# Kernel optimization log

Hardware: AMD Instinct MI355X
Metric: run time of the kernel (lower is better)

The kernel has to match this reference:

```python
import jax, jax.numpy as jnp
import numpy as np

D_IN = 1024
D_OUT = 1024


def setup_inputs() -> dict:
    key = jax.random.key(0)
    kx, kq, kk, kv = jax.random.split(key, 4)
    s = 1.0 / np.sqrt(D_IN)
    x = jax.random.normal(kx, (2, 4096, D_IN), dtype=jnp.float32)
    # nn.Linear weights: shape [d_out, d_in], y = x @ W.T (no bias)
    W_query = jax.random.normal(kq, (D_OUT, D_IN), dtype=jnp.float32) * s
    W_key = jax.random.normal(kk, (D_OUT, D_IN), dtype=jnp.float32) * s
    W_value = jax.random.normal(kv, (D_OUT, D_IN), dtype=jnp.float32) * s
    return {"x": x, "W_query": W_query, "W_key": W_key, "W_value": W_value}


def reference(x, W_query, W_key, W_value):
    # QKV projections: [b, n, d_in] @ [d_in, d_out]
    q = jnp.einsum('bnd,od->bno', x, W_query)
    k = jnp.einsum('bnd,od->bno', x, W_key)
    v = jnp.einsum('bnd,od->bno', x, W_value)
    d_k = k.shape[-1]
    scores = jnp.einsum('bqo,bko->bqk', q, k) / jnp.sqrt(jnp.asarray(d_k, x.dtype))
    # NOTE: source applies no causal mask despite the class name
    attn = jax.nn.softmax(scores, axis=-1)
    return jnp.einsum('bqk,bko->bqo', attn, v)
```

## Files before the change

kernel.cpp:

```cpp
#include <hip/hip_runtime.h>
#include <hip/hip_bf16.h>
#include <hip/hip_fp16.h>
#include <stdint.h>

typedef __bf16 bf16_t;
typedef __bf16 bf16x8 __attribute__((ext_vector_type(8)));
typedef float f32x4 __attribute__((ext_vector_type(4)));

typedef __attribute__((address_space(1))) void gv_t;
typedef __attribute__((address_space(3))) void lv_t;

__device__ inline unsigned short f2bf_bits(float f) {
  uint32_t u = __float_as_uint(f);
  u += 0x7FFFu + ((u >> 16) & 1u);
  return (unsigned short)(u >> 16);
}
__device__ inline bf16_t f2bf(float f) {
  unsigned short h = f2bf_bits(f);
  return __builtin_bit_cast(bf16_t, h);
}

__device__ inline void storeC(float* p, float v) { *p = v; }
__device__ inline void storeC(bf16_t* p, float v) { *p = f2bf(v); }
__device__ inline void storeC(__half* p, float v) { *p = __float2half(v); }

__global__ __launch_bounds__(256)
void convert_all(const float* __restrict__ x, const float* __restrict__ wq,
                 const float* __restrict__ wk, const float* __restrict__ wv,
                 bf16_t* __restrict__ xb, bf16_t* __restrict__ wqkb,
                 bf16_t* __restrict__ wvb)
{
  const int64_t NX = 8192LL * 1024, NW = 1024LL * 1024;
  const int64_t total4 = (NX + 3 * NW) >> 2;
  for (int64_t i = (int64_t)blockIdx.x * blockDim.x + threadIdx.x; i < total4;
       i += (int64_t)gridDim.x * blockDim.x) {
    int64_t e = i << 2;
    const float* src; bf16_t* dst; int64_t off;
    if (e < NX)               { src = x;  dst = xb;         off = e; }
    else if (e < NX + NW)     { src = wq; dst = wqkb;       off = e - NX; }
    else if (e < NX + 2 * NW) { src = wk; dst = wqkb + NW;  off = e - NX - NW; }
    else                      { src = wv; dst = wvb;        off = e - NX - 2 * NW; }
    float4 f = *(const float4*)(src + off);
    uint32_t lo = ((uint32_t)f2bf_bits(f.y) << 16) | f2bf_bits(f.x);
    uint32_t hi = ((uint32_t)f2bf_bits(f.w) << 16) | f2bf_bits(f.z);
    *(uint2*)(dst + off) = make_uint2(lo, hi);
  }
}

template <typename OUT_T>
__global__ __launch_bounds__(256)
void gemm_bt(const bf16_t* __restrict__ A, const bf16_t* __restrict__ B,
             OUT_T* __restrict__ C, int K, int lda, int ldb, int ldc,
             int64_t b_batch_stride, int bm_per_batch)
{
  __shared__ bf16_t As[2][128 * 32];
  __shared__ bf16_t Bs[2][128 * 32];
  const int tid  = threadIdx.x;
  const int wid  = tid >> 6;
  const int lane = tid & 63;
  const int wm = wid >> 1, wn = wid & 1;
  const int64_t bm = blockIdx.x;
  const int64_t bn = blockIdx.y;

  const bf16_t* Bb = B + (bm / bm_per_batch) * b_batch_stride;

  const int c0row = (wid * 2 + 0) * 16 + (lane >> 2);
  const int c1row = (wid * 2 + 1) * 16 + (lane >> 2);
  const int scol  = (lane & 3) * 8;

  const bf16_t* Ar0 = A  + (bm * 128 + c0row) * lda + scol;
  const bf16_t* Ar1 = A  + (bm * 128 + c1row) * lda + scol;
  const bf16_t* Br0 = Bb + (bn * 128 + c0row) * ldb + scol;
  const bf16_t* Br1 = Bb + (bn * 128 + c1row) * ldb + scol;

  const int ad0 = (wid * 2 + 0) * 512;
  const int ad1 = (wid * 2 + 1) * 512;

  const int frow = lane & 15;
  const int fk   = (lane >> 4) * 8;
  const int aoff = (wm * 64 + frow) * 32 + fk;
  const int boff = (wn * 64 + frow) * 32 + fk;

  f32x4 acc[4][4];
  #pragma unroll
  for (int m = 0; m < 4; m++)
    #pragma unroll
    for (int n = 0; n < 4; n++) acc[m][n] = f32x4{0.f, 0.f, 0.f, 0.f};

  auto stage = [&](int buf, int k0) {
    __builtin_amdgcn_global_load_lds((const gv_t*)(Ar0 + k0),
                                     (lv_t*)(&As[buf][ad0]), 16, 0, 0);
    __builtin_amdgcn_global_load_lds((const gv_t*)(Ar1 + k0),
                                     (lv_t*)(&As[buf][ad1]), 16, 0, 0);
    __builtin_amdgcn_global_load_lds((const gv_t*)(Br0 + k0),
                                     (lv_t*)(&Bs[buf][ad0]), 16, 0, 0);
    __builtin_amdgcn_global_load_lds((const gv_t*)(Br1 + k0),
                                     (lv_t*)(&Bs[buf][ad1]), 16, 0, 0);
  };

  stage(0, 0);
  __syncthreads();
  int cur = 0;
  for (int k0 = 0; k0 < K; k0 += 32) {
    if (k0 + 32 < K) stage(cur ^ 1, k0 + 32);

    bf16x8 af[4], bfr[4];
    #pragma unroll
    for (int m = 0; m < 4; m++)
      af[m] = *(const bf16x8*)(&As[cur][aoff + m * 16 * 32]);
    #pragma unroll
    for (int n = 0; n < 4; n++)
      bfr[n] = *(const bf16x8*)(&Bs[cur][boff + n * 16 * 32]);
    #pragma unroll
    for (int m = 0; m < 4; m++)
      #pragma unroll
      for (int n = 0; n < 4; n++)
        acc[m][n] = __builtin_amdgcn_mfma_f32_16x16x32_bf16(af[m], bfr[n],
                                                            acc[m][n], 0, 0, 0);
    __syncthreads();
    cur ^= 1;
  }

  const int crow = (lane >> 4) * 4;
  const int ccol = lane & 15;
  #pragma unroll
  for (int m = 0; m < 4; m++)
    #pragma unroll
    for (int n = 0; n < 4; n++)
      #pragma unroll
      for (int j = 0; j < 4; j++) {
        int64_t row = bm * 128 + wm * 64 + m * 16 + crow + j;
        int64_t col = bn * 128 + wn * 64 + n * 16 + ccol;
        storeC(&C[row * ldc + col], acc[m][n][j]);
      }
}

template <typename OUT_T>
__global__ __launch_bounds__(512, 2)
void gemm256(const bf16_t* __restrict__ A, const bf16_t* __restrict__ B,
             OUT_T* __restrict__ C0, OUT_T* __restrict__ C1,
             int K, int lda, int ldb, int ldc,
             int64_t b_batch_stride, int bm_per_batch,
             int64_t za_off, int64_t zb_off)
{
  __shared__ bf16_t As[2][256][64];
  __shared__ bf16_t Bs[2][256][64];

  const int tid  = threadIdx.x;
  const int wid  = tid >> 6;
  const int lane = tid & 63;
  const int wm = wid >> 2;
  const int wn = wid & 3;
  const int64_t bm = blockIdx.x;
  const int64_t bn = blockIdx.y;
  const int z = blockIdx.z;

  OUT_T* __restrict__ C = (z == 0) ? C0 : C1;
  const bf16_t* Ap = A + (int64_t)z * za_off;
  const bf16_t* Bp = B + (bm / bm_per_batch) * b_batch_stride
                       + (int64_t)z * zb_off;

  const int srow  = wid * 16 + (lane >> 3);
  const int sslot = (lane & 7) ^ (lane >> 3);
  const int64_t lda64 = lda, ldb64 = ldb;
  const bf16_t* Ag = Ap + (bm * 256 + srow) * lda64 + sslot * 8;
  const bf16_t* Bg = Bp + (bn * 256 + srow) * ldb64 + sslot * 8;

  auto stageA = [&](int buf, int t, int h) {
    const bf16_t* src = Ag + (int64_t)(h * 128) * lda64 + t * 64;
    char* dst = (char*)&As[buf][h * 128 + wid * 16][0];
    __builtin_amdgcn_global_load_lds((const gv_t*)src, (lv_t*)dst, 16, 0, 0);
    __builtin_amdgcn_global_load_lds((const gv_t*)(src + 8 * lda64),
                                     (lv_t*)(dst + 1024), 16, 0, 0);
  };
  auto stageB = [&](int buf, int t, int h) {
    const bf16_t* src = Bg + (int64_t)(h * 128) * ldb64 + t * 64;
    char* dst = (char*)&Bs[buf][h * 128 + wid * 16][0];
    __builtin_amdgcn_global_load_lds((const gv_t*)src, (lv_t*)dst, 16, 0, 0);
    __builtin_amdgcn_global_load_lds((const gv_t*)(src + 8 * ldb64),
                                     (lv_t*)(dst + 1024), 16, 0, 0);
  };

  const int frow   = lane & 15;
  const int fcol16 = lane >> 4;
  const int xorv   = (lane & 7) << 4;
  const int ck0 = (fcol16 * 16) ^ xorv;
  const int ck1 = (64 + fcol16 * 16) ^ xorv;
  const int arowb = (wm * 128 + frow) * 128;
  const int browb = (wn * 64  + frow) * 128;

  f32x4 acc[8][4];
  #pragma unroll
  for (int m = 0; m < 8; m++)
    #pragma unroll
    for (int n = 0; n < 4; n++) acc[m][n] = f32x4{0.f, 0.f, 0.f, 0.f};

  const int NT = K >> 6;

  stageA(0, 0, 0); stageA(0, 0, 1);
  stageB(0, 0, 0); stageB(0, 0, 1);
  stageB(1, 1, 0); stageB(1, 1, 1);
  asm volatile("s_waitcnt vmcnt(4)" ::: "memory");
  __builtin_amdgcn_s_barrier();
  __builtin_amdgcn_sched_barrier(0);

  bf16x8 a[4][2], bb[4][2];

  for (int g = 0; g < NT; ++g) {
    const int buf = g & 1;
    const char* lA = (const char*)&As[buf][0][0];
    const char* lB = (const char*)&Bs[buf][0][0];

    #pragma unroll
    for (int m = 0; m < 4; m++) {
      a[m][0] = *(const bf16x8*)(lA + arowb + m * 2048 + ck0);
      a[m][1] = *(const bf16x8*)(lA + arowb + m * 2048 + ck1);
    }
    #pragma unroll
    for (int n = 0; n < 2; n++) {
      bb[n][0] = *(const bf16x8*)(lB + browb + n * 2048 + ck0);
      bb[n][1] = *(const bf16x8*)(lB + browb + n * 2048 + ck1);
    }
    if (g + 1 < NT) stageA(buf ^ 1, g + 1, 0);
    __builtin_amdgcn_s_barrier();
    __builtin_amdgcn_s_setprio(1);
    #pragma unroll
    for (int m = 0; m < 4; m++)
      #pragma unroll
      for (int n = 0; n < 2; n++)
        #pragma unroll
        for (int k = 0; k < 2; k++)
          acc[m][n] = __builtin_amdgcn_mfma_f32_16x16x32_bf16(a[m][k], bb[n][k],
                                                              acc[m][n], 0, 0, 0);
    __builtin_amdgcn_s_setprio(0);
    __builtin_amdgcn_s_barrier();

    #pragma unroll
    for (int n = 2; n < 4; n++) {
      bb[n][0] = *(const bf16x8*)(lB + browb + n * 2048 + ck0);
      bb[n][1] = *(const bf16x8*)(lB + browb + n * 2048 + ck1);
    }
    if (g + 1 < NT) stageA(buf ^ 1, g + 1, 1);
    __builtin_amdgcn_s_barrier();
    __builtin_amdgcn_s_setprio(1);
    #pragma unroll
    for (int m = 0; m < 4; m++)
      #pragma unroll
      for (int n = 2; n < 4; n++)
        #pragma unroll
        for (int k = 0; k < 2; k++)
          acc[m][n] = __builtin_amdgcn_mfma_f32_16x16x32_bf16(a[m][k], bb[n][k],
                                                              acc[m][n], 0, 0, 0);
    __builtin_amdgcn_s_setprio(0);
    __builtin_amdgcn_s_barrier();

    #pragma unroll
    for (int m = 0; m < 4; m++) {
      a[m][0] = *(const bf16x8*)(lA + arowb + (m + 4) * 2048 + ck0);
      a[m][1] = *(const bf16x8*)(lA + arowb + (m + 4) * 2048 + ck1);
    }
    if (g + 2 < NT) stageB(buf, g + 2, 0);
    __builtin_amdgcn_s_barrier();
    __builtin_amdgcn_s_setprio(1);
    #pragma unroll
    for (int m = 0; m < 4; m++)
      #pragma unroll
      for (int n = 0; n < 2; n++)
        #pragma unroll
        for (int k = 0; k < 2; k++)
          acc[m + 4][n] = __builtin_amdgcn_mfma_f32_16x16x32_bf16(
              a[m][k], bb[n][k], acc[m + 4][n], 0, 0, 0);
    __builtin_amdgcn_s_setprio(0);
    __builtin_amdgcn_s_barrier();

    if (g + 2 < NT) stageB(buf, g + 2, 1);
    __builtin_amdgcn_s_barrier();
    __builtin_amdgcn_s_setprio(1);
    #pragma unroll
    for (int m = 0; m < 4; m++)
      #pragma unroll
      for (int n = 2; n < 4; n++)
        #pragma unroll
        for (int k = 0; k < 2; k++)
          acc[m + 4][n] = __builtin_amdgcn_mfma_f32_16x16x32_bf16(
              a[m][k], bb[n][k], acc[m + 4][n], 0, 0, 0);
    __builtin_amdgcn_s_setprio(0);
    if (g + 2 < NT) {
      asm volatile("s_waitcnt vmcnt(4)" ::: "memory");
    } else {
      asm volatile("s_waitcnt vmcnt(0)" ::: "memory");
    }
    __builtin_amdgcn_s_barrier();
    __builtin_amdgcn_sched_barrier(0);
  }

  const int crow = (lane >> 4) * 4;
  const int ccol = lane & 15;
  #pragma unroll
  for (int m = 0; m < 8; m++)
    #pragma unroll
    for (int n = 0; n < 4; n++)
      #pragma unroll
      for (int j = 0; j < 4; j++) {
        int64_t row = bm * 256 + wm * 128 + m * 16 + crow + j;
        int64_t col = bn * 256 + wn * 64 + n * 16 + ccol;
        storeC(&C[row * (int64_t)ldc + col], acc[m][n][j]);
      }
}

__global__ __launch_bounds__(256)
void softmax_rows(__half* __restrict__ SP)
{
  const int64_t row = blockIdx.x;
  __half* s = SP + row * 4096;
  bf16_t* p = (bf16_t*)s;
  const int tid = threadIdx.x;
  const float scale = 0.03125f;

  float v[16];
  float vmax = -3.4e38f;
  #pragma unroll
  for (int i = 0; i < 4; i++) {
    uint2 raw = *(const uint2*)(s + i * 1024 + tid * 4);
    __half2 h01 = __builtin_bit_cast(__half2, raw.x);
    __half2 h23 = __builtin_bit_cast(__half2, raw.y);
    float2 f01 = __half22float2(h01);
    float2 f23 = __half22float2(h23);
    v[i * 4 + 0] = f01.x * scale;
    v[i * 4 + 1] = f01.y * scale;
    v[i * 4 + 2] = f23.x * scale;
    v[i * 4 + 3] = f23.y * scale;
    vmax = fmaxf(vmax, fmaxf(fmaxf(v[i*4+0], v[i*4+1]),
                             fmaxf(v[i*4+2], v[i*4+3])));
  }
  #pragma unroll
  for (int o = 32; o > 0; o >>= 1) vmax = fmaxf(vmax, __shfl_xor(vmax, o));
  __shared__ float redm[4];
  __shared__ float reds[4];
  if ((tid & 63) == 0) redm[tid >> 6] = vmax;
  __syncthreads();
  vmax = fmaxf(fmaxf(redm[0], redm[1]), fmaxf(redm[2], redm[3]));

  float lsum = 0.f;
  #pragma unroll
  for (int i = 0; i < 16; i++) {
    v[i] = __expf(v[i] - vmax);
    lsum += v[i];
  }
  #pragma unroll
  for (int o = 32; o > 0; o >>= 1) lsum += __shfl_xor(lsum, o);
  if ((tid & 63) == 0) reds[tid >> 6] = lsum;
  __syncthreads();
  lsum = (reds[0] + reds[1]) + (reds[2] + reds[3]);
  const float inv = 1.0f / lsum;

  #pragma unroll
  for (int i = 0; i < 4; i++) {
    uint32_t lo = ((uint32_t)f2bf_bits(v[i*4+1] * inv) << 16) | f2bf_bits(v[i*4+0] * inv);
    uint32_t hi = ((uint32_t)f2bf_bits(v[i*4+3] * inv) << 16) | f2bf_bits(v[i*4+2] * inv);
    *(uint2*)(p + i * 1024 + tid * 4) = make_uint2(lo, hi);
  }
}

__global__ __launch_bounds__(256)
void addk_f4(float4* __restrict__ o, const float4* __restrict__ a, int64_t n4)
{
  for (int64_t i = (int64_t)blockIdx.x * blockDim.x + threadIdx.x; i < n4;
       i += (int64_t)gridDim.x * blockDim.x) {
    float4 x = o[i];
    float4 y = a[i];
    x.x += y.x; x.y += y.y; x.z += y.z; x.w += y.w;
    o[i] = x;
  }
}

extern "C" void kernel_launch(void* const* d_in, const int* in_sizes, int n_in,
                              void* d_out, int out_size, void* d_ws, size_t ws_size,
                              hipStream_t stream) {
  const float* x  = (const float*)d_in[0];
  const float* wq = (const float*)d_in[1];
  const float* wk = (const float*)d_in[2];
  const float* wv = (const float*)d_in[3];
  float* out = (float*)d_out;

  char* ws = (char*)d_ws;
  bf16_t* xb   = (bf16_t*)ws;
  bf16_t* wqkb = (bf16_t*)(ws + (16LL << 20));
  bf16_t* wvb  = (bf16_t*)(ws + (20LL << 20));
  __half* S    = (__half*)ws;
  bf16_t* qk   = (bf16_t*)(ws + (64LL << 20));
  float*  pk   = (float*)(ws + (64LL << 20));
  bf16_t* vt   = (bf16_t*)(ws + (96LL << 20));

  const int NO_BATCH = 1 << 30;

  convert_all<<<2048, 256, 0, stream>>>(x, wq, wk, wv, xb, wqkb, wvb);

  gemm256<bf16_t><<<dim3(32, 8, 1), 512, 0, stream>>>(
      xb, wqkb, qk, qk, 1024, 1024, 1024, 2048, 0, NO_BATCH, 0, 0);

  gemm_bt<bf16_t><<<dim3(8, 64), 256, 0, stream>>>(
      wvb, xb, vt, 1024, 1024, 1024, 8192, 0, NO_BATCH);

  gemm256<__half><<<dim3(32, 16, 1), 512, 0, stream>>>(
      qk, qk + 1024, S, S, 1024, 2048, 2048, 4096, 4096LL * 2048, 16, 0, 0);

  softmax_rows<<<8192, 256, 0, stream>>>(S);

  gemm256<float><<<dim3(32, 4, 2), 512, 0, stream>>>(
      (const bf16_t*)S, vt, out, pk, 2048, 4096, 8192, 1024,
      4096, 16, 2048, 2048);

  addk_f4<<<2048, 256, 0, stream>>>((float4*)out, (const float4*)pk,
                                    8192LL * 1024 / 4);
}
```

Baseline: 249.0 us.

## Hoist all LDS fragment loads per k-step and store split-K partial as fp16

Each gemm256 k-iteration now loads all eight A fragments and all four B fragments from LDS at the start, instead of interleaving smaller loads between MFMA phases. This doubles the fragment registers held per thread but removes mid-iteration LDS waits. Separately, the second split-K partial of the PV GEMM is written as fp16 rather than fp32, and the reduction kernel converts it back. That halves that buffer's write and read traffic at the cost of some precision in the partial sum.

```diff
diff --git a/kernel.cpp b/kernel.cpp
--- a/kernel.cpp
+++ b/kernel.cpp
@@ -135,10 +135,10 @@
       }
 }
 
-template <typename OUT_T>
+template <typename OUT_T, typename OUT2_T>
 __global__ __launch_bounds__(512, 2)
 void gemm256(const bf16_t* __restrict__ A, const bf16_t* __restrict__ B,
-             OUT_T* __restrict__ C0, OUT_T* __restrict__ C1,
+             OUT_T* __restrict__ C0, OUT2_T* __restrict__ C1,
              int K, int lda, int ldb, int ldc,
              int64_t b_batch_stride, int bm_per_batch,
              int64_t za_off, int64_t zb_off)
@@ -155,7 +155,6 @@
   const int64_t bn = blockIdx.y;
   const int z = blockIdx.z;
 
-  OUT_T* __restrict__ C = (z == 0) ? C0 : C1;
   const bf16_t* Ap = A + (int64_t)z * za_off;
   const bf16_t* Bp = B + (bm / bm_per_batch) * b_batch_stride
                        + (int64_t)z * zb_off;
@@ -204,7 +203,7 @@
   __builtin_amdgcn_s_barrier();
   __builtin_amdgcn_sched_barrier(0);
 
-  bf16x8 a[4][2], bb[4][2];
+  bf16x8 a[8][2], bb[4][2];
 
   for (int g = 0; g < NT; ++g) {
     const int buf = g & 1;
@@ -212,12 +211,12 @@
     const char* lB = (const char*)&Bs[buf][0][0];
 
     #pragma unroll
-    for (int m = 0; m < 4; m++) {
+    for (int m = 0; m < 8; m++) {
       a[m][0] = *(const bf16x8*)(lA + arowb + m * 2048 + ck0);
       a[m][1] = *(const bf16x8*)(lA + arowb + m * 2048 + ck1);
     }
     #pragma unroll
-    for (int n = 0; n < 2; n++) {
+    for (int n = 0; n < 4; n++) {
       bb[n][0] = *(const bf16x8*)(lB + browb + n * 2048 + ck0);
       bb[n][1] = *(const bf16x8*)(lB + browb + n * 2048 + ck1);
     }
@@ -235,11 +234,6 @@
     __builtin_amdgcn_s_setprio(0);
     __builtin_amdgcn_s_barrier();
 
-    #pragma unroll
-    for (int n = 2; n < 4; n++) {
-      bb[n][0] = *(const bf16x8*)(lB + browb + n * 2048 + ck0);
-      bb[n][1] = *(const bf16x8*)(lB + browb + n * 2048 + ck1);
-    }
     if (g + 1 < NT) stageA(buf ^ 1, g + 1, 1);
     __builtin_amdgcn_s_barrier();
     __builtin_amdgcn_s_setprio(1);
@@ -254,22 +248,17 @@
     __builtin_amdgcn_s_setprio(0);
     __builtin_amdgcn_s_barrier();
 
-    #pragma unroll
-    for (int m = 0; m < 4; m++) {
-      a[m][0] = *(const bf16x8*)(lA + arowb + (m + 4) * 2048 + ck0);
-      a[m][1] = *(const bf16x8*)(lA + arowb + (m + 4) * 2048 + ck1);
-    }
     if (g + 2 < NT) stageB(buf, g + 2, 0);
     __builtin_amdgcn_s_barrier();
     __builtin_amdgcn_s_setprio(1);
     #pragma unroll
-    for (int m = 0; m < 4; m++)
+    for (int m = 4; m < 8; m++)
       #pragma unroll
       for (int n = 0; n < 2; n++)
         #pragma unroll
         for (int k = 0; k < 2; k++)
-          acc[m + 4][n] = __builtin_amdgcn_mfma_f32_16x16x32_bf16(
-              a[m][k], bb[n][k], acc[m + 4][n], 0, 0, 0);
+          acc[m][n] = __builtin_amdgcn_mfma_f32_16x16x32_bf16(
+              a[m][k], bb[n][k], acc[m][n], 0, 0, 0);
     __builtin_amdgcn_s_setprio(0);
     __builtin_amdgcn_s_barrier();
 
@@ -277,13 +266,13 @@
     __builtin_amdgcn_s_barrier();
     __builtin_amdgcn_s_setprio(1);
     #pragma unroll
-    for (int m = 0; m < 4; m++)
+    for (int m = 4; m < 8; m++)
       #pragma unroll
       for (int n = 2; n < 4; n++)
         #pragma unroll
         for (int k = 0; k < 2; k++)
-          acc[m + 4][n] = __builtin_amdgcn_mfma_f32_16x16x32_bf16(
-              a[m][k], bb[n][k], acc[m + 4][n], 0, 0, 0);
+          acc[m][n] = __builtin_amdgcn_mfma_f32_16x16x32_bf16(
+              a[m][k], bb[n][k], acc[m][n], 0, 0, 0);
     __builtin_amdgcn_s_setprio(0);
     if (g + 2 < NT) {
       asm volatile("s_waitcnt vmcnt(4)" ::: "memory");
@@ -296,16 +285,29 @@
 
   const int crow = (lane >> 4) * 4;
   const int ccol = lane & 15;
-  #pragma unroll
-  for (int m = 0; m < 8; m++)
-    #pragma unroll
-    for (int n = 0; n < 4; n++)
-      #pragma unroll
-      for (int j = 0; j < 4; j++) {
-        int64_t row = bm * 256 + wm * 128 + m * 16 + crow + j;
-        int64_t col = bn * 256 + wn * 64 + n * 16 + ccol;
-        storeC(&C[row * (int64_t)ldc + col], acc[m][n][j]);
-      }
+  if (z == 0) {
+    #pragma unroll
+    for (int m = 0; m < 8; m++)
+      #pragma unroll
+      for (int n = 0; n < 4; n++)
+        #pragma unroll
+        for (int j = 0; j < 4; j++) {
+          int64_t row = bm * 256 + wm * 128 + m * 16 + crow + j;
+          int64_t col = bn * 256 + wn * 64 + n * 16 + ccol;
+          storeC(&C0[row * (int64_t)ldc + col], acc[m][n][j]);
+        }
+  } else {
+    #pragma unroll
+    for (int m = 0; m < 8; m++)
+      #pragma unroll
+      for (int n = 0; n < 4; n++)
+        #pragma unroll
+        for (int j = 0; j < 4; j++) {
+          int64_t row = bm * 256 + wm * 128 + m * 16 + crow + j;
+          int64_t col = bn * 256 + wn * 64 + n * 16 + ccol;
+          storeC(&C1[row * (int64_t)ldc + col], acc[m][n][j]);
+        }
+  }
 }
 
 __global__ __launch_bounds__(256)
@@ -363,13 +365,17 @@
 }
 
 __global__ __launch_bounds__(256)
-void addk_f4(float4* __restrict__ o, const float4* __restrict__ a, int64_t n4)
+void addk_h4(float4* __restrict__ o, const uint2* __restrict__ a, int64_t n4)
 {
   for (int64_t i = (int64_t)blockIdx.x * blockDim.x + threadIdx.x; i < n4;
        i += (int64_t)gridDim.x * blockDim.x) {
     float4 x = o[i];
-    float4 y = a[i];
-    x.x += y.x; x.y += y.y; x.z += y.z; x.w += y.w;
+    uint2 raw = a[i];
+    __half2 h01 = __builtin_bit_cast(__half2, raw.x);
+    __half2 h23 = __builtin_bit_cast(__half2, raw.y);
+    float2 f01 = __half22float2(h01);
+    float2 f23 = __half22float2(h23);
+    x.x += f01.x; x.y += f01.y; x.z += f23.x; x.w += f23.y;
     o[i] = x;
   }
 }
@@ -389,28 +395,28 @@
   bf16_t* wvb  = (bf16_t*)(ws + (20LL << 20));
   __half* S    = (__half*)ws;
   bf16_t* qk   = (bf16_t*)(ws + (64LL << 20));
-  float*  pk   = (float*)(ws + (64LL << 20));
+  __half* pk16 = (__half*)(ws + (64LL << 20));
   bf16_t* vt   = (bf16_t*)(ws + (96LL << 20));
 
   const int NO_BATCH = 1 << 30;
 
   convert_all<<<2048, 256, 0, stream>>>(x, wq, wk, wv, xb, wqkb, wvb);
 
-  gemm256<bf16_t><<<dim3(32, 8, 1), 512, 0, stream>>>(
+  gemm256<bf16_t, bf16_t><<<dim3(32, 8, 1), 512, 0, stream>>>(
       xb, wqkb, qk, qk, 1024, 1024, 1024, 2048, 0, NO_BATCH, 0, 0);
 
   gemm_bt<bf16_t><<<dim3(8, 64), 256, 0, stream>>>(
       wvb, xb, vt, 1024, 1024, 1024, 8192, 0, NO_BATCH);
 
-  gemm256<__half><<<dim3(32, 16, 1), 512, 0, stream>>>(
+  gemm256<__half, __half><<<dim3(32, 16, 1), 512, 0, stream>>>(
       qk, qk + 1024, S, S, 1024, 2048, 2048, 4096, 4096LL * 2048, 16, 0, 0);
 
   softmax_rows<<<8192, 256, 0, stream>>>(S);
 
-  gemm256<float><<<dim3(32, 4, 2), 512, 0, stream>>>(
-      (const bf16_t*)S, vt, out, pk, 2048, 4096, 8192, 1024,
+  gemm256<float, __half><<<dim3(32, 4, 2), 512, 0, stream>>>(
+      (const bf16_t*)S, vt, out, pk16, 2048, 4096, 8192, 1024,
       4096, 16, 2048, 2048);
 
-  addk_f4<<<2048, 256, 0, stream>>>((float4*)out, (const float4*)pk,
+  addk_h4<<<2048, 256, 0, stream>>>((float4*)out, (const uint2*)pk16,
                                     8192LL * 1024 / 4);
 }
```

Measured after the change: 247.3 us. About the same (-0.7%).
